# Optimization experiments

Hardware: AMD Instinct MI355X
Metric: run time of the kernel (lower is better)

Reference implementation:

```python
import jax, jax.numpy as jnp
import numpy as np

K = 1  # top-k from init_kwargs


def setup_inputs() -> dict:
    key = jax.random.key(0)
    k0, k1, k2, k3, k4, k5 = jax.random.split(key, 6)
    B, L, Ed, NE = 8192, 1024, 1024, 8
    D = L + Ed  # input_dim = latent_dim + embed_dim
    s = 1.0 / np.sqrt(D)  # torch nn.Linear default init bound
    x = jax.random.normal(k0, (B, L), dtype=jnp.float32)
    y = jax.random.normal(k1, (B, Ed), dtype=jnp.float32)
    We = jax.random.uniform(k2, (NE, D, D), dtype=jnp.float32, minval=-s, maxval=s)  # expert weights [E, out, in]
    be = jax.random.uniform(k3, (NE, D), dtype=jnp.float32, minval=-s, maxval=s)
    gW = jax.random.uniform(k4, (NE, D), dtype=jnp.float32, minval=-s, maxval=s)  # gate weight [E, in]
    gb = jax.random.uniform(k5, (NE,), dtype=jnp.float32, minval=-s, maxval=s)
    return {"x": x, "y": y, "We": We, "be": be, "gW": gW, "gb": gb}


def reference(x, y, We, be, gW, gb):
    # inp: [B, D]
    inp = jnp.concatenate([x, y], axis=1)
    # gate logits: [B, E] (eval mode: no noise)
    gate_logits = inp @ gW.T + gb
    topk_val, topk_idx = jax.lax.top_k(gate_logits, K)  # [B, K]
    topk_gates = jax.nn.softmax(topk_val, axis=1)       # [B, K]
    # dense compute-all-experts (faithful to original): [B, E, D]
    all_out = jnp.einsum('bd,eod->beo', inp, We) + be[None, :, :]
    # gather top-k experts per token: [B, K, D]
    gathered = jnp.take_along_axis(all_out, topk_idx[:, :, None], axis=1)
    fused = jnp.sum(gathered * topk_gates[:, :, None], axis=1)  # [B, D]
    return fused
```

## Files before the change

### kernel.cpp

```cpp
#include <hip/hip_runtime.h>
#include <stdint.h>

#define B_TOK 8192
#define DIM   2048
#define NE    8
#define BM 128
#define BN 128
#define BK 64

typedef __bf16 bf16x8 __attribute__((ext_vector_type(8)));
typedef float  f32x4  __attribute__((ext_vector_type(4)));

__device__ __forceinline__ unsigned short f2b(float f) {
  unsigned u = __builtin_bit_cast(unsigned, f);
  u += 0x7fffu + ((u >> 16) & 1u);
  return (unsigned short)(u >> 16);
}
__device__ __forceinline__ uint2 pack4(float4 v) {
  uint2 r;
  r.x = (unsigned)f2b(v.x) | ((unsigned)f2b(v.y) << 16);
  r.y = (unsigned)f2b(v.z) | ((unsigned)f2b(v.w) << 16);
  return r;
}
__device__ __forceinline__ void gload16(const void* g, void* l) {
  __builtin_amdgcn_global_load_lds(
      (const __attribute__((address_space(1))) void*)g,
      (__attribute__((address_space(3))) void*)l, 16, 0, 0);
}

__global__ __launch_bounds__(256) void cvt_we(const float* __restrict__ src,
                                              unsigned short* __restrict__ dst) {
  size_t idx = (size_t)blockIdx.x * 256 + threadIdx.x;
  float4 v = *(const float4*)(src + idx * 4);
  *(uint2*)(dst + idx * 4) = pack4(v);
}

template <bool WINP>
__global__ void gate_kernel(const float* __restrict__ x,
                            const float* __restrict__ y,
                            const float* __restrict__ gW,
                            const float* __restrict__ gb,
                            int* __restrict__ eid,
                            unsigned short* __restrict__ inpB) {
  const int tid = threadIdx.x;
  const int ln = tid & 63;
  const int token = blockIdx.x * 4 + (tid >> 6);

  double acc[NE];
#pragma unroll
  for (int e = 0; e < NE; ++e) acc[e] = 0.0;

  const float* bases[2] = {x, y};
#pragma unroll
  for (int p = 0; p < 2; ++p) {
    const float* rowp = bases[p] + (size_t)token * 1024;
#pragma unroll
    for (int it = 0; it < 4; ++it) {
      const int d = it * 256 + ln * 4;
      float4 v = *(const float4*)(rowp + d);
      if (WINP)
        *(uint2*)(inpB + (size_t)token * DIM + p * 1024 + d) = pack4(v);
#pragma unroll
      for (int e = 0; e < NE; ++e) {
        float4 g = *(const float4*)(gW + e * DIM + p * 1024 + d);
        acc[e] += (double)v.x * (double)g.x + (double)v.y * (double)g.y +
                  (double)v.z * (double)g.z + (double)v.w * (double)g.w;
      }
    }
  }
#pragma unroll
  for (int e = 0; e < NE; ++e) {
#pragma unroll
    for (int off = 32; off >= 1; off >>= 1) acc[e] += __shfl_xor(acc[e], off, 64);
  }
  if (ln == 0) {
    int best = 0;
    double bv = acc[0] + (double)gb[0];
#pragma unroll
    for (int e = 1; e < NE; ++e) {
      double v = acc[e] + (double)gb[e];
      if (v > bv) { bv = v; best = e; }
    }
    eid[token] = best;
  }
}

__global__ __launch_bounds__(256) void bucketize(const int* __restrict__ eid,
                                                 int* __restrict__ counts,
                                                 int* __restrict__ perm) {
  const int e = blockIdx.x;
  const int tid = threadIdx.x, ln = tid & 63, wv = tid >> 6;
  __shared__ int wsum[4];
  __shared__ int basev;
  if (tid == 0) basev = 0;
  __syncthreads();
  for (int t0 = 0; t0 < B_TOK; t0 += 256) {
    int t = t0 + tid;
    bool m = (eid[t] == e);
    unsigned long long mk = __ballot(m);
    int pre = __popcll(mk & ((1ull << ln) - 1ull));
    if (ln == 0) wsum[wv] = __popcll(mk);
    __syncthreads();
    int off = basev;
    for (int w = 0; w < wv; ++w) off += wsum[w];
    if (m) perm[e * B_TOK + off + pre] = t;
    __syncthreads();
    if (tid == 0) basev += wsum[0] + wsum[1] + wsum[2] + wsum[3];
    __syncthreads();
  }
  if (tid == 0) counts[e] = basev;
}

template <bool PRE>
__global__ __launch_bounds__(256) void moe_gemm(
    const float* __restrict__ x,
    const float* __restrict__ y,
    const float* __restrict__ We,
    const float* __restrict__ be,
    const unsigned short* __restrict__ inpB,
    const unsigned short* __restrict__ WeB,
    const int* __restrict__ counts,
    const int* __restrict__ perm,
    float* __restrict__ out) {
  __shared__ unsigned short As[BM * BK];
  __shared__ unsigned short Bs[BN * BK];
  __shared__ int tokLds[BM];

  const int e = blockIdx.z;
  const int cnt = counts[e];
  const int m0 = blockIdx.y * BM;
  if (m0 >= cnt) return;
  const int n0 = blockIdx.x * BN;

  const int tid = threadIdx.x;
  const int ln = tid & 63;
  const int wv = tid >> 6;
  const int wm = wv & 1, wn = wv >> 1;

  if (tid < BM) {
    int r = m0 + tid;
    tokLds[tid] = perm[e * B_TOK + (r < cnt ? r : cnt - 1)];
  }
  __syncthreads();

  const int cS = (ln & 7) ^ ((ln >> 3) & 7);
  int tokA[4], rowB[4];
#pragma unroll
  for (int j = 0; j < 4; ++j) {
    int row = (wv * 4 + j) * 8 + (ln >> 3);
    tokA[j] = tokLds[row];
    rowB[j] = row;
  }
  const unsigned short* wbbase = WeB + (size_t)e * DIM * DIM;
  const float* wfbase = We + (size_t)e * DIM * DIM;

  f32x4 acc[4][4];
#pragma unroll
  for (int i = 0; i < 4; ++i)
#pragma unroll
    for (int j = 0; j < 4; ++j) acc[i][j] = (f32x4){0.f, 0.f, 0.f, 0.f};

  for (int k0 = 0; k0 < DIM; k0 += BK) {
    __syncthreads();
    if constexpr (PRE) {
#pragma unroll
      for (int j = 0; j < 4; ++j) {
        gload16(inpB + (size_t)tokA[j] * DIM + k0 + cS * 8,
                &As[(wv * 4 + j) * 512]);
        gload16(wbbase + (size_t)(n0 + rowB[j]) * DIM + k0 + cS * 8,
                &Bs[(wv * 4 + j) * 512]);
      }
    } else {
      const float* ab = (k0 < 1024) ? x : y;
      const int kk = k0 & 1023;
#pragma unroll
      for (int i = 0; i < 8; ++i) {
        int li = i * 256 + tid;
        int row = li >> 4, k4 = li & 15;
        int ksl = (k4 & 7) ^ (row & 7);
        int chunk = k4 >> 1, half = k4 & 1;
        int slot = (chunk ^ (row & 7)) * 2 + half;
        int tok = tokLds[row];
        float4 va = *(const float4*)(ab + (size_t)tok * 1024 + kk + k4 * 4);
        *(uint2*)&As[row * BK + slot * 4] = pack4(va);
        float4 vb = *(const float4*)(wfbase + (size_t)(n0 + row) * DIM + k0 + k4 * 4);
        *(uint2*)&Bs[row * BK + slot * 4] = pack4(vb);
        (void)ksl;
      }
    }
    __syncthreads();

#pragma unroll
    for (int ks = 0; ks < 2; ++ks) {
      bf16x8 av[4], bv[4];
#pragma unroll
      for (int i = 0; i < 4; ++i) {
        int rA = wm * 64 + i * 16 + (ln & 15);
        int c = ks * 4 + (ln >> 4);
        av[i] = *(const bf16x8*)&As[rA * BK + (c ^ (rA & 7)) * 8];
      }
#pragma unroll
      for (int j = 0; j < 4; ++j) {
        int rB = wn * 64 + j * 16 + (ln & 15);
        int c = ks * 4 + (ln >> 4);
        bv[j] = *(const bf16x8*)&Bs[rB * BK + (c ^ (rB & 7)) * 8];
      }
#pragma unroll
      for (int i = 0; i < 4; ++i)
#pragma unroll
        for (int j = 0; j < 4; ++j)
          acc[i][j] = __builtin_amdgcn_mfma_f32_16x16x32_bf16(av[i], bv[j], acc[i][j], 0, 0, 0);
    }
  }

  float bias[4]; int col[4];
#pragma unroll
  for (int j = 0; j < 4; ++j) {
    col[j] = n0 + wn * 64 + j * 16 + (ln & 15);
    bias[j] = be[e * DIM + col[j]];
  }
#pragma unroll
  for (int i = 0; i < 4; ++i) {
    int rbase = wm * 64 + i * 16 + ((ln >> 4) << 2);
#pragma unroll
    for (int r = 0; r < 4; ++r) {
      int rl = rbase + r;
      if (m0 + rl < cnt) {
        size_t t = (size_t)tokLds[rl];
#pragma unroll
        for (int j = 0; j < 4; ++j)
          out[t * DIM + col[j]] = acc[i][j][r] + bias[j];
      }
    }
  }
}

extern "C" void kernel_launch(void* const* d_in, const int* in_sizes, int n_in,
                              void* d_out, int out_size, void* d_ws, size_t ws_size,
                              hipStream_t stream) {
  const float* x  = (const float*)d_in[0];
  const float* y  = (const float*)d_in[1];
  const float* We = (const float*)d_in[2];
  const float* be = (const float*)d_in[3];
  const float* gW = (const float*)d_in[4];
  const float* gb = (const float*)d_in[5];
  float* out = (float*)d_out;

  char* ws = (char*)d_ws;
  int* counts = (int*)ws;
  int* eid    = (int*)(ws + 256);
  int* perm   = (int*)(ws + 33024);
  unsigned short* inpB = (unsigned short*)(ws + 295168);
  unsigned short* WeB  = (unsigned short*)(ws + 33849600);
  const size_t needed = 33849600ull + 67108864ull;

  if (ws_size >= needed) {
    gate_kernel<true><<<dim3(B_TOK / 4), 256, 0, stream>>>(x, y, gW, gb, eid, inpB);
    cvt_we<<<dim3(32768), 256, 0, stream>>>(We, WeB);
    bucketize<<<dim3(NE), 256, 0, stream>>>(eid, counts, perm);
    moe_gemm<true><<<dim3(DIM / BN, B_TOK / BM, NE), 256, 0, stream>>>(
        x, y, We, be, inpB, WeB, counts, perm, out);
  } else {
    gate_kernel<false><<<dim3(B_TOK / 4), 256, 0, stream>>>(x, y, gW, gb, eid, nullptr);
    bucketize<<<dim3(NE), 256, 0, stream>>>(eid, counts, perm);
    moe_gemm<false><<<dim3(DIM / BN, B_TOK / BM, NE), 256, 0, stream>>>(
        x, y, We, be, nullptr, nullptr, counts, perm, out);
  }
}
```

Baseline: 433.9 us.

## Fuse gating, weight conversion, and bucketing into one pre-pass kernel

Merges the gate kernel, the expert-weight bf16 conversion and the bucketize kernel into a single launch. Blocks are split by index into gating work and conversion work, and the serial per-expert bucketize scan is replaced by atomicAdd slot allocation into the per-expert permutation lists. A memset zeroes the counts first. This removes two launches and the single-block-per-expert scan, but token order within each expert becomes nondeterministic, which may hurt locality of the gathered rows.

```diff
diff --git a/kernel.cpp b/kernel.cpp
--- a/kernel.cpp
+++ b/kernel.cpp
@@ -7,6 +7,8 @@
 #define BM 128
 #define BN 128
 #define BK 64
+#define GATE_BLOCKS 2048
+#define CVT_BLOCKS  8192
 
 typedef __bf16 bf16x8 __attribute__((ext_vector_type(8)));
 typedef float  f32x4  __attribute__((ext_vector_type(4)));
@@ -28,23 +30,34 @@
       (__attribute__((address_space(3))) void*)l, 16, 0, 0);
 }
 
-__global__ __launch_bounds__(256) void cvt_we(const float* __restrict__ src,
-                                              unsigned short* __restrict__ dst) {
-  size_t idx = (size_t)blockIdx.x * 256 + threadIdx.x;
-  float4 v = *(const float4*)(src + idx * 4);
-  *(uint2*)(dst + idx * 4) = pack4(v);
-}
-
-template <bool WINP>
-__global__ void gate_kernel(const float* __restrict__ x,
-                            const float* __restrict__ y,
-                            const float* __restrict__ gW,
-                            const float* __restrict__ gb,
-                            int* __restrict__ eid,
-                            unsigned short* __restrict__ inpB) {
+template <bool FULL>
+__global__ __launch_bounds__(256) void fused_pre(
+    const float* __restrict__ x,
+    const float* __restrict__ y,
+    const float* __restrict__ gW,
+    const float* __restrict__ gb,
+    const float* __restrict__ We,
+    int* __restrict__ counts,
+    int* __restrict__ perm,
+    unsigned short* __restrict__ inpB,
+    unsigned short* __restrict__ WeB) {
+  const int bid = blockIdx.x;
+
+  if (FULL && bid >= GATE_BLOCKS) {
+    const int cb = bid - GATE_BLOCKS;
+    const size_t base = (size_t)cb * 1024;
+#pragma unroll
+    for (int j = 0; j < 4; ++j) {
+      size_t i4 = base + (size_t)(j * 256 + threadIdx.x);
+      float4 v = *(const float4*)(We + i4 * 4);
+      *(uint2*)(WeB + i4 * 4) = pack4(v);
+    }
+    return;
+  }
+
   const int tid = threadIdx.x;
   const int ln = tid & 63;
-  const int token = blockIdx.x * 4 + (tid >> 6);
+  const int token = bid * 4 + (tid >> 6);
 
   double acc[NE];
 #pragma unroll
@@ -58,7 +71,7 @@
     for (int it = 0; it < 4; ++it) {
       const int d = it * 256 + ln * 4;
       float4 v = *(const float4*)(rowp + d);
-      if (WINP)
+      if (FULL)
         *(uint2*)(inpB + (size_t)token * DIM + p * 1024 + d) = pack4(v);
 #pragma unroll
       for (int e = 0; e < NE; ++e) {
@@ -81,34 +94,9 @@
       double v = acc[e] + (double)gb[e];
       if (v > bv) { bv = v; best = e; }
     }
-    eid[token] = best;
-  }
-}
-
-__global__ __launch_bounds__(256) void bucketize(const int* __restrict__ eid,
-                                                 int* __restrict__ counts,
-                                                 int* __restrict__ perm) {
-  const int e = blockIdx.x;
-  const int tid = threadIdx.x, ln = tid & 63, wv = tid >> 6;
-  __shared__ int wsum[4];
-  __shared__ int basev;
-  if (tid == 0) basev = 0;
-  __syncthreads();
-  for (int t0 = 0; t0 < B_TOK; t0 += 256) {
-    int t = t0 + tid;
-    bool m = (eid[t] == e);
-    unsigned long long mk = __ballot(m);
-    int pre = __popcll(mk & ((1ull << ln) - 1ull));
-    if (ln == 0) wsum[wv] = __popcll(mk);
-    __syncthreads();
-    int off = basev;
-    for (int w = 0; w < wv; ++w) off += wsum[w];
-    if (m) perm[e * B_TOK + off + pre] = t;
-    __syncthreads();
-    if (tid == 0) basev += wsum[0] + wsum[1] + wsum[2] + wsum[3];
-    __syncthreads();
-  }
-  if (tid == 0) counts[e] = basev;
+    int slot = atomicAdd(&counts[best], 1);
+    perm[best * B_TOK + slot] = token;
+  }
 }
 
 template <bool PRE>
@@ -177,7 +165,6 @@
       for (int i = 0; i < 8; ++i) {
         int li = i * 256 + tid;
         int row = li >> 4, k4 = li & 15;
-        int ksl = (k4 & 7) ^ (row & 7);
         int chunk = k4 >> 1, half = k4 & 1;
         int slot = (chunk ^ (row & 7)) * 2 + half;
         int tok = tokLds[row];
@@ -185,7 +172,6 @@
         *(uint2*)&As[row * BK + slot * 4] = pack4(va);
         float4 vb = *(const float4*)(wfbase + (size_t)(n0 + row) * DIM + k0 + k4 * 4);
         *(uint2*)&Bs[row * BK + slot * 4] = pack4(vb);
-        (void)ksl;
       }
     }
     __syncthreads();
@@ -248,21 +234,21 @@
 
   char* ws = (char*)d_ws;
   int* counts = (int*)ws;
-  int* eid    = (int*)(ws + 256);
-  int* perm   = (int*)(ws + 33024);
-  unsigned short* inpB = (unsigned short*)(ws + 295168);
-  unsigned short* WeB  = (unsigned short*)(ws + 33849600);
-  const size_t needed = 33849600ull + 67108864ull;
+  int* perm   = (int*)(ws + 256);
+  unsigned short* inpB = (unsigned short*)(ws + 262400);
+  unsigned short* WeB  = (unsigned short*)(ws + 33816832);
+  const size_t needed = 33816832ull + 67108864ull;
+
+  hipMemsetAsync(counts, 0, 256, stream);
 
   if (ws_size >= needed) {
-    gate_kernel<true><<<dim3(B_TOK / 4), 256, 0, stream>>>(x, y, gW, gb, eid, inpB);
-    cvt_we<<<dim3(32768), 256, 0, stream>>>(We, WeB);
-    bucketize<<<dim3(NE), 256, 0, stream>>>(eid, counts, perm);
+    fused_pre<true><<<dim3(GATE_BLOCKS + CVT_BLOCKS), 256, 0, stream>>>(
+        x, y, gW, gb, We, counts, perm, inpB, WeB);
     moe_gemm<true><<<dim3(DIM / BN, B_TOK / BM, NE), 256, 0, stream>>>(
         x, y, We, be, inpB, WeB, counts, perm, out);
   } else {
-    gate_kernel<false><<<dim3(B_TOK / 4), 256, 0, stream>>>(x, y, gW, gb, eid, nullptr);
-    bucketize<<<dim3(NE), 256, 0, stream>>>(eid, counts, perm);
+    fused_pre<false><<<dim3(GATE_BLOCKS), 256, 0, stream>>>(
+        x, y, gW, gb, We, counts, perm, nullptr, nullptr);
     moe_gemm<false><<<dim3(DIM / BN, B_TOK / BM, NE), 256, 0, stream>>>(
         x, y, We, be, nullptr, nullptr, counts, perm, out);
   }
```

Result: slower. 470.4 us (+8.4%).
